# Kernel optimization log

Measured on AMD Instinct MI355X. Metric: run time of the kernel, lower is better.

The kernel has to match this reference:

```python
import jax, jax.numpy as jnp
import numpy as np

B, S, D = 4, 4096, 2048      # batch, seq, model_dim
E = 128                      # emb_dim (hardcoded in module)
H = 128                      # head_dim
TAU = 0.4                    # self.T
BASE = 3.0                   # self.base (gumbel-sigmoid offset)
LN_EPS = 1e-5


def setup_inputs() -> dict:
    key = jax.random.key(0)
    k_x, k_wr, k_wd, k_g = jax.random.split(key, 4)
    x = jax.random.normal(k_x, (B, S, D), dtype=jnp.float32)
    # torch nn.Linear stores weight as [out_features, in_features]
    W_router = jax.random.normal(k_wr, (E, D), dtype=jnp.float32) / np.sqrt(D)
    W_decoder = jax.random.normal(k_wd, (H, E), dtype=jnp.float32) / np.sqrt(E)
    ln_gamma = jnp.ones((E,), dtype=jnp.float32)
    ln_beta = jnp.zeros((E,), dtype=jnp.float32)
    rnn_state = jnp.zeros((E,), dtype=jnp.float32)  # registered buffer, zeros
    # torch: gumbels = -Exp(1).log()  -> standard Gumbel(0,1) noise
    u = jax.random.uniform(k_g, (B, S, H), dtype=jnp.float32, minval=1e-20, maxval=1.0)
    gumbel_noise = -jnp.log(-jnp.log(u))
    return {
        "x": x, "W_router": W_router, "W_decoder": W_decoder,
        "ln_gamma": ln_gamma, "ln_beta": ln_beta, "rnn_state": rnn_state,
        "gumbel_noise": gumbel_noise, "top_k": 32,
    }


def reference(x, W_router, W_decoder, ln_gamma, ln_beta, rnn_state, gumbel_noise, top_k):
    # router linear (no bias): [B,S,D] @ [D,E] -> [B,S,E]
    out = jnp.einsum("bsd,ed->bse", x, W_router)
    full_emb = rnn_state + out
    # LayerNorm over emb dim (biased variance, as torch LayerNorm)
    mu = full_emb.mean(-1, keepdims=True)
    var = full_emb.var(-1, keepdims=True)
    h = (full_emb - mu) / jnp.sqrt(var + LN_EPS) * ln_gamma + ln_beta
    # decoder linear after exact GELU: [B,S,E] @ [E,H] -> [B,S,H]
    logits = jnp.einsum("bse,he->bsh", jax.nn.gelu(h, approximate=False), W_decoder)
    # gumbel-sigmoid (soft): sigmoid((logits + gumbel + offset)/tau)
    binary_approx = jax.nn.sigmoid((logits + gumbel_noise + BASE) / TAU)
    # hard_sample: straight-through round
    binary = jax.lax.stop_gradient(jnp.round(binary_approx) - binary_approx) + binary_approx
    # top-k mask over head_dim
    _, topk_idx = jax.lax.top_k(binary_approx, top_k)            # [B,S,top_k]
    topk_mask = jax.nn.one_hot(topk_idx, H, dtype=binary_approx.dtype).sum(-2)  # [B,S,H]
    cnt = binary.sum(-1, keepdims=True)
    binary = jnp.where(cnt > top_k, topk_mask, binary)
    # fallback: if a token selects nothing, pick argmax of soft scores
    zero_mask = binary.sum(-1, keepdims=True) == 0
    fallback = jax.nn.one_hot(jnp.argmax(binary_approx, axis=-1), H, dtype=binary_approx.dtype)
    binary = jnp.where(zero_mask, fallback, binary)
    binary = binary.reshape(B, S, -1, H)  # [B,S,1,H]
    return binary, binary_approx
```

## Files before the change

### kernel.cpp

```cpp
#include <hip/hip_runtime.h>
#include <math.h>

#define NTOK   16384
#define DDIM   2048
#define EDIM   128
#define HDIM   128
#define TOKT   32
#define KC     32
#define NCH    (DDIM / KC)

typedef __attribute__((ext_vector_type(8))) _Float16 half8;
typedef __attribute__((ext_vector_type(4))) _Float16 half4;
typedef __attribute__((ext_vector_type(4))) float    f32x4;

__device__ __forceinline__ int swz(int t, int e) {
  return t * EDIM + ((e & 96) | ((e ^ t) & 31));
}

__global__ __launch_bounds__(256)
void conv_w(const float* __restrict__ Wr,
            _Float16* __restrict__ wh, _Float16* __restrict__ wl) {
  const int idx  = (int)blockIdx.x * 256 + (int)threadIdx.x;
  const int lane = idx & 63;
  const int ks   = (idx >> 6) & 63;
  const int nt   = idx >> 12;
  const int n    = nt * 16 + (lane & 15);
  const int k0   = ks * 32 + (lane >> 4) * 8;
  half8 h, l;
#pragma unroll
  for (int j = 0; j < 8; ++j) {
    const float w = Wr[(size_t)n * DDIM + k0 + j] * 32.0f;
    const _Float16 hh = (_Float16)w;
    h[j] = hh;
    l[j] = (_Float16)((w - (float)hh) * 2048.0f);
  }
  *(half8*)(wh + (size_t)idx * 8) = h;
  *(half8*)(wl + (size_t)idx * 8) = l;
}

__global__ __launch_bounds__(1024, 8)
void fused_router(const float* __restrict__ x,
                  const _Float16* __restrict__ wsh,
                  const _Float16* __restrict__ wsl,
                  const float* __restrict__ Wd,
                  const float* __restrict__ gamma,
                  const float* __restrict__ beta,
                  const float* __restrict__ rnn,
                  const float* __restrict__ gum,
                  float* __restrict__ outb,
                  float* __restrict__ outa) {
  __shared__ char smraw[40960];
  _Float16* const xs = (_Float16*)smraw;
  float* const A  = (float*)smraw;
  float* const G4 = (float*)(smraw + 16384);

  const int tid  = (int)threadIdx.x;
  const int wv   = __builtin_amdgcn_readfirstlane(tid >> 6);
  const int lane = tid & 63;
  const int t0   = (int)blockIdx.x * TOKT;

  const int nt   = wv & 7;
  const int mt   = wv >> 3;
  const int quad = lane >> 4;
  const int col  = lane & 15;

  const int offA = mt * 512 + lane * 8;
  const int offB = 4096 + nt * 1024 + lane * 8;

  const bool xstage = tid < 256;
  const int  sx_t   = tid >> 3;
  const int  sx_k8  = tid & 7;
  const float* xg   = x + (size_t)(t0 + sx_t) * DDIM + sx_k8 * 4;
  const int  sx_off = (sx_t >> 4) * 512 + (sx_k8 >> 1) * 128
                    + (sx_t & 15) * 8 + (sx_k8 & 1) * 4;

  const int wnt = wv & 7;
  const int wpl = wv >> 3;
  const _Float16* wsrc = (wpl ? wsl : wsh) + (size_t)wnt * 32768 + (size_t)lane * 8;
  const int sw_off = 4096 + wnt * 1024 + wpl * 512;

  f32x4 hh = {0,0,0,0}, cr = {0,0,0,0};

  __builtin_amdgcn_global_load_lds(
      (const __attribute__((address_space(1))) void*)wsrc,
      (__attribute__((address_space(3))) void*)(xs + sw_off),
      16, 0, 0);
  if (xstage) {
    const float4 a = *(const float4*)xg;
    half4 h4, l4;
#pragma unroll
    for (int m = 0; m < 4; ++m) {
      const float v = (&a.x)[m];
      const _Float16 hv = (_Float16)v;
      h4[m] = hv; l4[m] = (_Float16)((v - (float)hv) * 2048.0f);
    }
    *(half4*)&xs[sx_off] = h4;
    *(half4*)&xs[1024 + sx_off] = l4;
  }

  float4 px;
#pragma unroll 2
  for (int c = 0; c < NCH; ++c) {
    __syncthreads();
    const int b  = c & 1;
    const int bn = b ^ 1;
    if (c + 1 < NCH) {
      __builtin_amdgcn_global_load_lds(
          (const __attribute__((address_space(1))) void*)(wsrc + (size_t)(c + 1) * 512),
          (__attribute__((address_space(3))) void*)(xs + bn * 8192 + sw_off),
          16, 0, 0);
      if (xstage) px = *(const float4*)(xg + (c + 1) * KC);
    }
    const half8 ah = *(const half8*)&xs[b * 2048 + offA];
    const half8 al = *(const half8*)&xs[b * 2048 + 1024 + offA];
    const half8 bh = *(const half8*)&xs[b * 8192 + offB];
    const half8 bl = *(const half8*)&xs[b * 8192 + offB + 512];

    hh = __builtin_amdgcn_mfma_f32_16x16x32_f16(ah, bh, hh, 0, 0, 0);
    cr = __builtin_amdgcn_mfma_f32_16x16x32_f16(ah, bl, cr, 0, 0, 0);
    cr = __builtin_amdgcn_mfma_f32_16x16x32_f16(al, bh, cr, 0, 0, 0);

    if (c + 1 < NCH && xstage) {
      half4 h4, l4;
#pragma unroll
      for (int m = 0; m < 4; ++m) {
        const float v = (&px.x)[m];
        const _Float16 hv = (_Float16)v;
        h4[m] = hv; l4[m] = (_Float16)((v - (float)hv) * 2048.0f);
      }
      *(half4*)&xs[bn * 2048 + sx_off] = h4;
      *(half4*)&xs[bn * 2048 + 1024 + sx_off] = l4;
    }
  }
  __syncthreads();

  {
    const int e  = nt * 16 + col;
    const float rv = rnn[e];
#pragma unroll
    for (int r = 0; r < 4; ++r)
      A[swz(mt * 16 + quad * 4 + r, e)] =
          hh[r] * (1.0f / 32.0f) + cr[r] * (1.0f / 65536.0f) + rv;
  }
  __syncthreads();

  const int e0 = wv * 8;
  {
    const float gm0 = gamma[lane], gm1 = gamma[lane + 64];
    const float bt0 = beta[lane],  bt1 = beta[lane + 64];
    for (int tt = wv * 2; tt < wv * 2 + 2; ++tt) {
      const float v0 = A[swz(tt, lane)];
      const float v1 = A[swz(tt, lane + 64)];
      float s = v0 + v1;
#pragma unroll
      for (int m = 32; m; m >>= 1) s += __shfl_xor(s, m);
      const float mu = s * (1.0f / 128.0f);
      const float d0 = v0 - mu, d1 = v1 - mu;
      float q = d0 * d0 + d1 * d1;
#pragma unroll
      for (int m = 32; m; m >>= 1) q += __shfl_xor(q, m);
      const float rstd = 1.0f / sqrtf(q * (1.0f / 128.0f) + 1e-5f);
      const float h0v = d0 * rstd * gm0 + bt0;
      const float h1v = d1 * rstd * gm1 + bt1;
      const float g0 = 0.5f * h0v * (1.0f + erff(h0v * 0.70710678118654752f));
      const float g1 = 0.5f * h1v * (1.0f + erff(h1v * 0.70710678118654752f));
      G4[(tt * 32 + ((lane >> 2) ^ tt)) * 4 + (lane & 3)] = g0;
      G4[(tt * 32 + ((((lane + 64) >> 2)) ^ tt)) * 4 + ((lane + 64) & 3)] = g1;
    }
  }
  __syncthreads();

  {
    float acc2[4] = {0.0f, 0.0f, 0.0f, 0.0f};
    const int tokn  = lane & 31;
    const int rbase = e0 + (lane >> 5) * 4;
    const float4* wd4 = (const float4*)(Wd + (size_t)rbase * EDIM);
#pragma unroll 2
    for (int kg = 0; kg < EDIM / 4; ++kg) {
      const float4 gv = *(const float4*)&G4[(tokn * 32 + (kg ^ tokn)) * 4];
#pragma unroll
      for (int j = 0; j < 4; ++j) {
        const float4 w = wd4[(size_t)j * (EDIM / 4) + kg];
        acc2[j] = fmaf(gv.x, w.x,
                  fmaf(gv.y, w.y,
                  fmaf(gv.z, w.z,
                  fmaf(gv.w, w.w, acc2[j]))));
      }
    }
#pragma unroll
    for (int j = 0; j < 4; ++j) A[swz(tokn, rbase + j)] = acc2[j];
  }
  __syncthreads();

  for (int tt = wv * 2; tt < wv * 2 + 2; ++tt) {
    const size_t T = (size_t)(t0 + tt);
    const float l0 = A[swz(tt, lane)];
    const float l1 = A[swz(tt, lane + 64)];
    const float gn0 = gum[T * HDIM + lane];
    const float gn1 = gum[T * HDIM + lane + 64];
    const float z0 = (l0 + gn0 + 3.0f) * 2.5f;
    const float z1 = (l1 + gn1 + 3.0f) * 2.5f;
    const float ba0 = 1.0f / (1.0f + expf(-z0));
    const float ba1 = 1.0f / (1.0f + expf(-z1));
    const unsigned ub0 = __float_as_uint(ba0);
    const unsigned ub1 = __float_as_uint(ba1);
    const int r0 = ba0 > 0.5f;
    const int r1 = ba1 > 0.5f;
    const int cnt = __popcll(__ballot(r0)) + __popcll(__ballot(r1));
    float bin0, bin1;
    if (cnt > 32) {
      unsigned v = 0u;
#pragma unroll
      for (int b = 29; b >= 0; --b) {
        const unsigned cand = v | (1u << b);
        const int cc = __popcll(__ballot(ub0 >= cand)) + __popcll(__ballot(ub1 >= cand));
        if (cc >= 32) v = cand;
      }
      const int cgt = __popcll(__ballot(ub0 > v)) + __popcll(__ballot(ub1 > v));
      const int r = 32 - cgt;
      const unsigned long long t0b = __ballot(ub0 == v);
      const unsigned long long t1b = __ballot(ub1 == v);
      const int n0 = __popcll(t0b);
      const unsigned long long mlt = (1ull << lane) - 1ull;
      const int rk0 = __popcll(t0b & mlt);
      const int rk1 = n0 + __popcll(t1b & mlt);
      bin0 = (ub0 > v || (ub0 == v && rk0 < r)) ? 1.0f : 0.0f;
      bin1 = (ub1 > v || (ub1 == v && rk1 < r)) ? 1.0f : 0.0f;
    } else if (cnt == 0) {
      float m = fmaxf(ba0, ba1);
#pragma unroll
      for (int mm = 32; mm; mm >>= 1) m = fmaxf(m, __shfl_xor(m, mm));
      const unsigned long long e0b = __ballot(ba0 == m);
      const unsigned long long e1b = __ballot(ba1 == m);
      const int hstar = e0b ? (__ffsll((unsigned long long)e0b) - 1)
                            : (64 + __ffsll((unsigned long long)e1b) - 1);
      bin0 = (lane == hstar) ? 1.0f : 0.0f;
      bin1 = (lane + 64 == hstar) ? 1.0f : 0.0f;
    } else {
      bin0 = r0 ? 1.0f : 0.0f;
      bin1 = r1 ? 1.0f : 0.0f;
    }
    outb[T * HDIM + lane]      = bin0;
    outb[T * HDIM + lane + 64] = bin1;
    outa[T * HDIM + lane]      = ba0;
    outa[T * HDIM + lane + 64] = ba1;
  }
}

extern "C" void kernel_launch(void* const* d_in, const int* in_sizes, int n_in,
                              void* d_out, int out_size, void* d_ws, size_t ws_size,
                              hipStream_t stream) {
  (void)in_sizes; (void)n_in; (void)ws_size; (void)out_size;
  const float* x   = (const float*)d_in[0];
  const float* Wr  = (const float*)d_in[1];
  const float* Wd  = (const float*)d_in[2];
  const float* gm  = (const float*)d_in[3];
  const float* bt  = (const float*)d_in[4];
  const float* rnn = (const float*)d_in[5];
  const float* gum = (const float*)d_in[6];
  float* outb = (float*)d_out;
  float* outa = outb + (size_t)NTOK * HDIM;

  _Float16* wh = (_Float16*)d_ws;
  _Float16* wl = wh + (size_t)EDIM * DDIM;

  conv_w<<<dim3(128), dim3(256), 0, stream>>>(Wr, wh, wl);
  fused_router<<<dim3(NTOK / TOKT), dim3(1024), 0, stream>>>(
      x, wh, wl, Wd, gm, bt, rnn, gum, outb, outa);
}
```

Measured before the change: 271.8 us.

## Double token tile to 64, split K across waves with 4-stage LDS pipeline

Each block now processes 64 tokens instead of 32. Each wave computes a 2x2 grid of MFMA tiles, and the 16 waves split the K dimension into two halves whose partial sums are added in shared memory. Loading uses a 4-deep LDS ring buffer with manual waitcnt and barriers, and x conversion is spread across all threads. The aim is to raise reuse of the router weight tiles per block and to hide global load latency. The cost is 96KB of LDS per block, which lowers occupancy, plus an extra reduction step and more register pressure.

Measured after the change: 259.4 us. 1.05x faster.

```diff
diff --git a/kernel.cpp b/kernel.cpp
--- a/kernel.cpp
+++ b/kernel.cpp
@@ -5,13 +5,16 @@
 #define DDIM   2048
 #define EDIM   128
 #define HDIM   128
-#define TOKT   32
+#define TOKT   64
 #define KC     32
-#define NCH    (DDIM / KC)
+#define NCH    64
+#define BUFB   24576
 
 typedef __attribute__((ext_vector_type(8))) _Float16 half8;
-typedef __attribute__((ext_vector_type(4))) _Float16 half4;
+typedef __attribute__((ext_vector_type(2))) _Float16 half2v;
 typedef __attribute__((ext_vector_type(4))) float    f32x4;
+
+#define MFMA16 __builtin_amdgcn_mfma_f32_16x16x32_f16
 
 __device__ __forceinline__ int swz(int t, int e) {
   return t * EDIM + ((e & 96) | ((e ^ t) & 31));
@@ -38,7 +41,7 @@
   *(half8*)(wl + (size_t)idx * 8) = l;
 }
 
-__global__ __launch_bounds__(1024, 8)
+__global__ __launch_bounds__(1024, 4)
 void fused_router(const float* __restrict__ x,
                   const _Float16* __restrict__ wsh,
                   const _Float16* __restrict__ wsl,
@@ -49,98 +52,135 @@
                   const float* __restrict__ gum,
                   float* __restrict__ outb,
                   float* __restrict__ outa) {
-  __shared__ char smraw[40960];
-  _Float16* const xs = (_Float16*)smraw;
+  __shared__ char smraw[98304];
+  char* const sm = smraw;
   float* const A  = (float*)smraw;
-  float* const G4 = (float*)(smraw + 16384);
+  float* const G4 = (float*)(smraw + 32768);
 
   const int tid  = (int)threadIdx.x;
   const int wv   = __builtin_amdgcn_readfirstlane(tid >> 6);
   const int lane = tid & 63;
   const int t0   = (int)blockIdx.x * TOKT;
 
-  const int nt   = wv & 7;
-  const int mt   = wv >> 3;
+  const int mg   = (wv >> 2) & 1;
+  const int ng   = wv & 3;
+  const int kw   = wv >> 3;
   const int quad = lane >> 4;
   const int col  = lane & 15;
 
-  const int offA = mt * 512 + lane * 8;
-  const int offB = 4096 + nt * 1024 + lane * 8;
-
-  const bool xstage = tid < 256;
-  const int  sx_t   = tid >> 3;
-  const int  sx_k8  = tid & 7;
-  const float* xg   = x + (size_t)(t0 + sx_t) * DDIM + sx_k8 * 4;
-  const int  sx_off = (sx_t >> 4) * 512 + (sx_k8 >> 1) * 128
-                    + (sx_t & 15) * 8 + (sx_k8 & 1) * 4;
-
-  const int wnt = wv & 7;
-  const int wpl = wv >> 3;
+  const int t_g = tid >> 4;
+  const int u   = tid & 15;
+  const float* xg = x + (size_t)(t0 + t_g) * DDIM + u * 2;
+  const int xw_off = (t_g >> 4) * 2048
+                   + ((u >> 2) * 16 + (t_g & 15)) * 16 + (u & 3) * 4;
+
+  const int wnt = wv >> 1, wpl = wv & 1;
   const _Float16* wsrc = (wpl ? wsl : wsh) + (size_t)wnt * 32768 + (size_t)lane * 8;
-  const int sw_off = 4096 + wnt * 1024 + wpl * 512;
-
-  f32x4 hh = {0,0,0,0}, cr = {0,0,0,0};
-
-  __builtin_amdgcn_global_load_lds(
-      (const __attribute__((address_space(1))) void*)wsrc,
-      (__attribute__((address_space(3))) void*)(xs + sw_off),
-      16, 0, 0);
-  if (xstage) {
-    const float4 a = *(const float4*)xg;
-    half4 h4, l4;
-#pragma unroll
-    for (int m = 0; m < 4; ++m) {
-      const float v = (&a.x)[m];
-      const _Float16 hv = (_Float16)v;
-      h4[m] = hv; l4[m] = (_Float16)((v - (float)hv) * 2048.0f);
-    }
-    *(half4*)&xs[sx_off] = h4;
-    *(half4*)&xs[1024 + sx_off] = l4;
-  }
-
-  float4 px;
-#pragma unroll 2
-  for (int c = 0; c < NCH; ++c) {
-    __syncthreads();
-    const int b  = c & 1;
-    const int bn = b ^ 1;
-    if (c + 1 < NCH) {
-      __builtin_amdgcn_global_load_lds(
-          (const __attribute__((address_space(1))) void*)(wsrc + (size_t)(c + 1) * 512),
-          (__attribute__((address_space(3))) void*)(xs + bn * 8192 + sw_off),
-          16, 0, 0);
-      if (xstage) px = *(const float4*)(xg + (c + 1) * KC);
-    }
-    const half8 ah = *(const half8*)&xs[b * 2048 + offA];
-    const half8 al = *(const half8*)&xs[b * 2048 + 1024 + offA];
-    const half8 bh = *(const half8*)&xs[b * 8192 + offB];
-    const half8 bl = *(const half8*)&xs[b * 8192 + offB + 512];
-
-    hh = __builtin_amdgcn_mfma_f32_16x16x32_f16(ah, bh, hh, 0, 0, 0);
-    cr = __builtin_amdgcn_mfma_f32_16x16x32_f16(ah, bl, cr, 0, 0, 0);
-    cr = __builtin_amdgcn_mfma_f32_16x16x32_f16(al, bh, cr, 0, 0, 0);
-
-    if (c + 1 < NCH && xstage) {
-      half4 h4, l4;
-#pragma unroll
-      for (int m = 0; m < 4; ++m) {
-        const float v = (&px.x)[m];
-        const _Float16 hv = (_Float16)v;
-        h4[m] = hv; l4[m] = (_Float16)((v - (float)hv) * 2048.0f);
+  const int wdst = 8192 + wnt * 2048 + wpl * 1024;
+
+  const int aoff0 = (mg * 2 + 0) * 2048 + lane * 16;
+  const int aoff1 = (mg * 2 + 1) * 2048 + lane * 16;
+  const int boff0 = 8192 + (ng * 2 + 0) * 2048 + lane * 16;
+  const int boff1 = 8192 + (ng * 2 + 1) * 2048 + lane * 16;
+
+  f32x4 hh[2][2], cr[2][2];
+#pragma unroll
+  for (int mi = 0; mi < 2; ++mi)
+#pragma unroll
+    for (int ni = 0; ni < 2; ++ni) { hh[mi][ni] = (f32x4){0,0,0,0}; cr[mi][ni] = (f32x4){0,0,0,0}; }
+
+  float2 rx0, rx1, rx2, rx3;
+
+#define XLD(c)  (*(const float2*)(xg + (c) * KC))
+#define GLDS(c, bsel) __builtin_amdgcn_global_load_lds( \
+    (const __attribute__((address_space(1))) void*)(wsrc + (size_t)(c) * 512), \
+    (__attribute__((address_space(3))) void*)(sm + (bsel) * BUFB + wdst), 16, 0, 0)
+#define XCVT(c, RU) do { \
+    const float v0_ = (RU).x, v1_ = (RU).y; \
+    const _Float16 h0_ = (_Float16)v0_, h1_ = (_Float16)v1_; \
+    const _Float16 l0_ = (_Float16)((v0_ - (float)h0_) * 2048.0f); \
+    const _Float16 l1_ = (_Float16)((v1_ - (float)h1_) * 2048.0f); \
+    char* wb_ = sm + ((c) & 3) * BUFB + xw_off; \
+    *(half2v*)wb_ = (half2v){h0_, h1_}; \
+    *(half2v*)(wb_ + 1024) = (half2v){l0_, l1_}; \
+  } while (0)
+
+#define ITER(c, RL, RU) do { \
+    const int cf_ = ((c) + 3 < NCH) ? (c) + 3 : NCH - 1; \
+    RL = XLD(cf_); \
+    GLDS(cf_, ((c) + 3) & 3); \
+    if ((c) + 1 < NCH) XCVT((c) + 1, RU); \
+    if (((c) >> 5) == kw) { \
+      const char* bb_ = sm + ((c) & 3) * BUFB; \
+      const half8 ah0 = *(const half8*)(bb_ + aoff0); \
+      const half8 al0 = *(const half8*)(bb_ + aoff0 + 1024); \
+      const half8 ah1 = *(const half8*)(bb_ + aoff1); \
+      const half8 al1 = *(const half8*)(bb_ + aoff1 + 1024); \
+      const half8 bh0 = *(const half8*)(bb_ + boff0); \
+      const half8 bl0 = *(const half8*)(bb_ + boff0 + 1024); \
+      const half8 bh1 = *(const half8*)(bb_ + boff1); \
+      const half8 bl1 = *(const half8*)(bb_ + boff1 + 1024); \
+      hh[0][0] = MFMA16(ah0, bh0, hh[0][0], 0, 0, 0); \
+      cr[0][0] = MFMA16(ah0, bl0, cr[0][0], 0, 0, 0); \
+      cr[0][0] = MFMA16(al0, bh0, cr[0][0], 0, 0, 0); \
+      hh[0][1] = MFMA16(ah0, bh1, hh[0][1], 0, 0, 0); \
+      cr[0][1] = MFMA16(ah0, bl1, cr[0][1], 0, 0, 0); \
+      cr[0][1] = MFMA16(al0, bh1, cr[0][1], 0, 0, 0); \
+      hh[1][0] = MFMA16(ah1, bh0, hh[1][0], 0, 0, 0); \
+      cr[1][0] = MFMA16(ah1, bl0, cr[1][0], 0, 0, 0); \
+      cr[1][0] = MFMA16(al1, bh0, cr[1][0], 0, 0, 0); \
+      hh[1][1] = MFMA16(ah1, bh1, hh[1][1], 0, 0, 0); \
+      cr[1][1] = MFMA16(ah1, bl1, cr[1][1], 0, 0, 0); \
+      cr[1][1] = MFMA16(al1, bh1, cr[1][1], 0, 0, 0); \
+    } \
+    asm volatile("s_waitcnt vmcnt(4) lgkmcnt(0)" ::: "memory"); \
+    asm volatile("s_barrier" ::: "memory"); \
+  } while (0)
+
+  rx0 = XLD(0); GLDS(0, 0);
+  rx1 = XLD(1); GLDS(1, 1);
+  rx2 = XLD(2); GLDS(2, 2);
+  XCVT(0, rx0);
+  asm volatile("s_waitcnt vmcnt(4) lgkmcnt(0)" ::: "memory");
+  asm volatile("s_barrier" ::: "memory");
+
+  for (int cc = 0; cc < NCH; cc += 4) {
+    ITER(cc + 0, rx3, rx1);
+    ITER(cc + 1, rx0, rx2);
+    ITER(cc + 2, rx1, rx3);
+    ITER(cc + 3, rx2, rx0);
+  }
+  asm volatile("s_waitcnt vmcnt(0) lgkmcnt(0)" ::: "memory");
+  asm volatile("s_barrier" ::: "memory");
+
+  if (kw == 0) {
+#pragma unroll
+    for (int mi = 0; mi < 2; ++mi)
+#pragma unroll
+      for (int ni = 0; ni < 2; ++ni)
+#pragma unroll
+        for (int r = 0; r < 4; ++r) {
+          const int t = (mg * 2 + mi) * 16 + quad * 4 + r;
+          const int e = (ng * 2 + ni) * 16 + col;
+          A[swz(t, e)] = hh[mi][ni][r] * (1.0f / 32.0f)
+                       + cr[mi][ni][r] * (1.0f / 65536.0f);
+        }
+  }
+  __syncthreads();
+  if (kw == 1) {
+#pragma unroll
+    for (int mi = 0; mi < 2; ++mi)
+#pragma unroll
+      for (int ni = 0; ni < 2; ++ni) {
+        const int e = (ng * 2 + ni) * 16 + col;
+        const float rv = rnn[e];
+#pragma unroll
+        for (int r = 0; r < 4; ++r) {
+          const int t = (mg * 2 + mi) * 16 + quad * 4 + r;
+          A[swz(t, e)] += hh[mi][ni][r] * (1.0f / 32.0f)
+                        + cr[mi][ni][r] * (1.0f / 65536.0f) + rv;
+        }
       }
-      *(half4*)&xs[bn * 2048 + sx_off] = h4;
-      *(half4*)&xs[bn * 2048 + 1024 + sx_off] = l4;
-    }
-  }
-  __syncthreads();
-
-  {
-    const int e  = nt * 16 + col;
-    const float rv = rnn[e];
-#pragma unroll
-    for (int r = 0; r < 4; ++r)
-      A[swz(mt * 16 + quad * 4 + r, e)] =
-          hh[r] * (1.0f / 32.0f) + cr[r] * (1.0f / 65536.0f) + rv;
   }
   __syncthreads();
 
@@ -148,7 +188,7 @@
   {
     const float gm0 = gamma[lane], gm1 = gamma[lane + 64];
     const float bt0 = beta[lane],  bt1 = beta[lane + 64];
-    for (int tt = wv * 2; tt < wv * 2 + 2; ++tt) {
+    for (int tt = wv * 4; tt < wv * 4 + 4; ++tt) {
       const float v0 = A[swz(tt, lane)];
       const float v1 = A[swz(tt, lane + 64)];
       float s = v0 + v1;
@@ -164,22 +204,23 @@
       const float h1v = d1 * rstd * gm1 + bt1;
       const float g0 = 0.5f * h0v * (1.0f + erff(h0v * 0.70710678118654752f));
       const float g1 = 0.5f * h1v * (1.0f + erff(h1v * 0.70710678118654752f));
-      G4[(tt * 32 + ((lane >> 2) ^ tt)) * 4 + (lane & 3)] = g0;
-      G4[(tt * 32 + ((((lane + 64) >> 2)) ^ tt)) * 4 + ((lane + 64) & 3)] = g1;
+      const int e0a = lane, e1a = lane + 64;
+      G4[(tt * 32 + (((e0a >> 2) ^ (tt & 31)))) * 4 + (e0a & 3)] = g0;
+      G4[(tt * 32 + (((e1a >> 2) ^ (tt & 31)))) * 4 + (e1a & 3)] = g1;
     }
   }
   __syncthreads();
 
   {
-    float acc2[4] = {0.0f, 0.0f, 0.0f, 0.0f};
-    const int tokn  = lane & 31;
-    const int rbase = e0 + (lane >> 5) * 4;
-    const float4* wd4 = (const float4*)(Wd + (size_t)rbase * EDIM);
+    float acc2[8];
+#pragma unroll
+    for (int j = 0; j < 8; ++j) acc2[j] = 0.0f;
+    const float4* wd4 = (const float4*)(Wd + (size_t)e0 * EDIM);
 #pragma unroll 2
     for (int kg = 0; kg < EDIM / 4; ++kg) {
-      const float4 gv = *(const float4*)&G4[(tokn * 32 + (kg ^ tokn)) * 4];
-#pragma unroll
-      for (int j = 0; j < 4; ++j) {
+      const float4 gv = *(const float4*)&G4[(lane * 32 + (kg ^ (lane & 31))) * 4];
+#pragma unroll
+      for (int j = 0; j < 8; ++j) {
         const float4 w = wd4[(size_t)j * (EDIM / 4) + kg];
         acc2[j] = fmaf(gv.x, w.x,
                   fmaf(gv.y, w.y,
@@ -187,12 +228,13 @@
                   fmaf(gv.w, w.w, acc2[j]))));
       }
     }
-#pragma unroll
-    for (int j = 0; j < 4; ++j) A[swz(tokn, rbase + j)] = acc2[j];
+    __syncthreads();
+#pragma unroll
+    for (int j = 0; j < 8; ++j) A[swz(lane, e0 + j)] = acc2[j];
   }
   __syncthreads();
 
-  for (int tt = wv * 2; tt < wv * 2 + 2; ++tt) {
+  for (int tt = wv * 4; tt < wv * 4 + 4; ++tt) {
     const size_t T = (size_t)(t0 + tt);
     const float l0 = A[swz(tt, lane)];
     const float l1 = A[swz(tt, lane + 64)];
```
